# Optimization experiments

Measured on AMD Instinct MI355X. Metric: run time of the kernel, lower is better.

The kernel has to match this reference:

```python
import jax, jax.numpy as jnp
import numpy as np

B, L, D, H, NB = 8, 256, 128, 4, 2
HD = D // H
N_ITEMS, TIME_SPAN = 50000, 256
EPS = 1e-8
NEG = -(2.0 ** 32) + 1.0  # torch uses -2**32+1 padding value


def _ln(x, g, b):
    m = jnp.mean(x, -1, keepdims=True)
    v = jnp.mean((x - m) ** 2, -1, keepdims=True)
    return (x - m) / jnp.sqrt(v + EPS) * g + b


def setup_inputs() -> dict:
    ks = iter(jax.random.split(jax.random.key(0), 40))

    def nrm(shape, s=0.02):
        return jax.random.normal(next(ks), shape, jnp.float32) * s

    inp = {
        "user_ids": jax.random.randint(next(ks), (B,), 0, 1000),
        "log_seqs": jax.random.randint(next(ks), (B, L), 0, N_ITEMS + 1),
        "time_matrices": jax.random.randint(next(ks), (B, L, L), 0, TIME_SPAN + 1),
        "pos_seqs": jax.random.randint(next(ks), (B, L), 1, N_ITEMS + 1),
        "neg_seqs": jax.random.randint(next(ks), (B, L), 1, N_ITEMS + 1),
    }
    inp["item_emb"] = nrm((N_ITEMS + 1, D)).at[0].set(0.0)  # padding_idx=0
    inp["posK_emb"] = nrm((L, D))
    inp["posV_emb"] = nrm((L, D))
    inp["timeK_emb"] = nrm((TIME_SPAN + 1, D))
    inp["timeV_emb"] = nrm((TIME_SPAN + 1, D))
    inp["ln1_g"] = jnp.ones((NB, D)); inp["ln1_b"] = jnp.zeros((NB, D))
    inp["Wq"] = nrm((NB, D, D)); inp["bq"] = jnp.zeros((NB, D))
    inp["Wk"] = nrm((NB, D, D)); inp["bk"] = jnp.zeros((NB, D))
    inp["Wv"] = nrm((NB, D, D)); inp["bv"] = jnp.zeros((NB, D))
    inp["ln2_g"] = jnp.ones((NB, D)); inp["ln2_b"] = jnp.zeros((NB, D))
    inp["W1"] = nrm((NB, D, D)); inp["b1"] = jnp.zeros((NB, D))
    inp["W2"] = nrm((NB, D, D)); inp["b2"] = jnp.zeros((NB, D))
    inp["lnf_g"] = jnp.ones((D,)); inp["lnf_b"] = jnp.zeros((D,))
    return inp


def reference(user_ids, log_seqs, time_matrices, pos_seqs, neg_seqs,
              item_emb, posK_emb, posV_emb, timeK_emb, timeV_emb,
              ln1_g, ln1_b, Wq, bq, Wk, bk, Wv, bv, ln2_g, ln2_b,
              W1, b1, W2, b2, lnf_g, lnf_b):
    # dropout layers are identity in eval mode
    seqs = item_emb[log_seqs] * jnp.sqrt(jnp.float32(D))          # [B,L,D]
    tK = timeK_emb[time_matrices].reshape(B, L, L, H, HD)          # [B,Lq,Lk,H,hd]
    tV = timeV_emb[time_matrices].reshape(B, L, L, H, HD)
    pad = log_seqs == 0                                            # [B,L]
    seqs = seqs * (~pad)[..., None]
    causal = jnp.triu(jnp.ones((L, L), bool), 1)                   # ~tril -> masked
    # time_mask masks by QUERY position (matches torch unsqueeze(-1).expand)
    mask = pad[:, None, :, None] | causal[None, None]              # [B,1,Lq,Lk]
    posKh = posK_emb.reshape(L, H, HD)
    posVh = posV_emb.reshape(L, H, HD)
    for i in range(NB):
        q_in = _ln(seqs, ln1_g[i], ln1_b[i])
        Qh = (q_in @ Wq[i] + bq[i]).reshape(B, L, H, HD).transpose(0, 2, 1, 3)
        Kh = (seqs @ Wk[i] + bk[i]).reshape(B, L, H, HD).transpose(0, 2, 1, 3)
        Vh = (seqs @ Wv[i] + bv[i]).reshape(B, L, H, HD).transpose(0, 2, 1, 3)
        scores = jnp.einsum("bhqd,bhkd->bhqk", Qh, Kh)
        scores = scores + jnp.einsum("bhqd,khd->bhqk", Qh, posKh)
        scores = scores + jnp.einsum("bqkhd,bhqd->bhqk", tK, Qh)
        scores = scores / jnp.sqrt(jnp.float32(HD))
        scores = jnp.where(mask, NEG, scores)
        A = jax.nn.softmax(scores, axis=-1)                        # [B,H,Lq,Lk]
        out = jnp.einsum("bhqk,bhkd->bhqd", A, Vh)
        out = out + jnp.einsum("bhqk,khd->bhqd", A, posVh)
        out = out + jnp.einsum("bhqk,bqkhd->bhqd", A, tV)
        out = out.transpose(0, 2, 1, 3).reshape(B, L, D)
        seqs = q_in + out                                          # residual on Q
        seqs = _ln(seqs, ln2_g[i], ln2_b[i])
        h = jax.nn.relu(seqs @ W1[i] + b1[i])                      # conv1d k=1 == linear
        seqs = seqs + (h @ W2[i] + b2[i])
        seqs = seqs * (~pad)[..., None]
    feats = _ln(seqs, lnf_g, lnf_b)
    pos_logits = jnp.sum(feats * item_emb[pos_seqs], -1)           # [B,L]
    neg_logits = jnp.sum(feats * item_emb[neg_seqs], -1)
    return (pos_logits, neg_logits)
```

## Files before the change

kernel.cpp:

```cpp
#include <hip/hip_runtime.h>
#include <hip/hip_bf16.h>

#define L_ 256
#define H_ 4
#define ROWS 2048
#define NEGV (-4294967295.0f)

typedef unsigned short us16;

__device__ __forceinline__ float us2f(us16 u){ return __uint_as_float(((unsigned)u)<<16); }
__device__ __forceinline__ us16 f2us(float f){ __hip_bfloat16 h=__float2bfloat16(f); return *(us16*)&h; }

struct KArgs {
    const int *log_seqs, *tmat, *pos_seqs, *neg_seqs;
    const float *item_emb, *posK, *posV, *timeK, *timeV;
    const float *ln1g, *ln1b, *bq, *bk, *bv, *ln2g, *ln2b, *b1, *b2, *lnfg, *lnfb;
    const float *Wq, *Wk, *Wv, *W1, *W2;
    float *qin0, *qin1, *out;
    us16 *wsW, *tmK, *tmV, *Qb0, *Kb0, *Vb0, *Qb1, *Kb1, *Vb1;
};

__device__ __forceinline__ void ln_rows(float* sA,
        const float* __restrict__ g, const float* __restrict__ b,
        float* qin_out, int r0, int tid){
    int r=tid>>5, l=tid&31;
    float* x=sA+r*128;
    float x0=x[l],x1=x[l+32],x2=x[l+64],x3=x[l+96];
    float s=x0+x1+x2+x3;
    #pragma unroll
    for(int o=16;o;o>>=1) s+=__shfl_xor(s,o,64);
    float m=s*(1.f/128.f);
    float d0=x0-m,d1=x1-m,d2=x2-m,d3=x3-m;
    float v=d0*d0+d1*d1+d2*d2+d3*d3;
    #pragma unroll
    for(int o=16;o;o>>=1) v+=__shfl_xor(v,o,64);
    float rstd=rsqrtf(v*(1.f/128.f)+1e-8f);
    float y0=d0*rstd*g[l]+b[l];
    float y1=d1*rstd*g[l+32]+b[l+32];
    float y2=d2*rstd*g[l+64]+b[l+64];
    float y3=d3*rstd*g[l+96]+b[l+96];
    x[l]=y0; x[l+32]=y1; x[l+64]=y2; x[l+96]=y3;
    if(qin_out){
        float* q=qin_out+(size_t)(r0+r)*128;
        q[l]=y0; q[l+32]=y1; q[l+64]=y2; q[l+96]=y3;
    }
}

__device__ __forceinline__ void gemm2x2(const float* A, const us16* sW,
        int ra, int rb, int c0, float* acc){
    float a00=0,a01=0,a10=0,a11=0;
    const float* Ar=A+ra*128;
    const float* Br=A+rb*128;
    #pragma unroll 8
    for(int k=0;k<128;k++){
        ushort2 wp=*(const ushort2*)(sW+k*128+c0);
        float w0=us2f(wp.x), w1=us2f(wp.y);
        float x0=Ar[k], x1=Br[k];
        a00=fmaf(x0,w0,a00); a01=fmaf(x0,w1,a01);
        a10=fmaf(x1,w0,a10); a11=fmaf(x1,w1,a11);
    }
    acc[0]=a00; acc[1]=a01; acc[2]=a10; acc[3]=a11;
}

__global__ __launch_bounds__(256) void k_pre(KArgs a){
    __shared__ __align__(16) char smem[36864];
    int tid=threadIdx.x, bid=blockIdx.x;
    if(bid<768){
        us16* sW=(us16*)smem;
        float* sA=(float*)(smem+32768);
        int m=bid>>8, rg=bid&255, r0=rg*8;
        {
            int rl=tid>>5, c4=tid&31;
            int id=a.log_seqs[r0+rl];
            float4 v=((const float4*)a.item_emb)[id*32+c4];
            float sc = id? 11.3137085f : 0.f;
            v.x*=sc; v.y*=sc; v.z*=sc; v.w*=sc;
            ((float4*)sA)[tid]=v;
        }
        const float* Wsrc=(m==0)?a.Wq:(m==1)?a.Wk:a.Wv;
        {
            const float4* src=(const float4*)Wsrc;
            ushort4* dst=(ushort4*)sW;
            #pragma unroll
            for(int j=0;j<16;j++){
                float4 w=src[j*256+tid];
                ushort4 o; o.x=f2us(w.x);o.y=f2us(w.y);o.z=f2us(w.z);o.w=f2us(w.w);
                dst[j*256+tid]=o;
            }
        }
        __syncthreads();
        if(m==0){ ln_rows(sA, a.ln1g, a.ln1b, a.qin0, r0, tid); __syncthreads(); }
        int cp=tid&63, rp=tid>>6, c0=2*cp, ra=2*rp, rb=ra+1;
        float acc[4];
        gemm2x2(sA,sW,ra,rb,c0,acc);
        if(m==0){
            float b0v=a.bq[c0], b1v=a.bq[c0+1];
            ushort2 s0; s0.x=f2us(acc[0]+b0v); s0.y=f2us(acc[1]+b1v);
            ushort2 s1; s1.x=f2us(acc[2]+b0v); s1.y=f2us(acc[3]+b1v);
            *(ushort2*)(a.Qb0+(size_t)(r0+ra)*128+c0)=s0;
            *(ushort2*)(a.Qb0+(size_t)(r0+rb)*128+c0)=s1;
        } else {
            const float* bb=(m==1)?a.bk:a.bv;
            const float* pp=(m==1)?a.posK:a.posV;
            us16* Oo=(m==1)?a.Kb0:a.Vb0;
            int qa=(r0+ra)&255, qb2=(r0+rb)&255;
            float b0v=bb[c0], b1v=bb[c0+1];
            ushort2 s0; s0.x=f2us(acc[0]+b0v+pp[qa*128+c0]);  s0.y=f2us(acc[1]+b1v+pp[qa*128+c0+1]);
            ushort2 s1; s1.x=f2us(acc[2]+b0v+pp[qb2*128+c0]); s1.y=f2us(acc[3]+b1v+pp[qb2*128+c0+1]);
            *(ushort2*)(Oo+(size_t)(r0+ra)*128+c0)=s0;
            *(ushort2*)(Oo+(size_t)(r0+rb)*128+c0)=s1;
        }
    } else if(bid<880){
        int j=bid-768; int m=j>>4; int idx=(j&15)*256+tid;
        const float* base;
        switch(m){
            case 0: base=a.W1; break;        case 1: base=a.W2; break;
            case 2: base=a.Wq+16384; break;  case 3: base=a.Wk+16384; break;
            case 4: base=a.Wv+16384; break;  case 5: base=a.W1+16384; break;
            default: base=a.W2+16384; break;
        }
        float4 v=((const float4*)base)[idx];
        ushort4 o; o.x=f2us(v.x);o.y=f2us(v.y);o.z=f2us(v.z);o.w=f2us(v.w);
        ((ushort4*)(a.wsW+(size_t)m*16384))[idx]=o;
    } else {
        int gi=(bid-880)*256+tid;
        if(gi<8224){
            float4 v=((const float4*)a.timeK)[gi];
            ushort4 o; o.x=f2us(v.x);o.y=f2us(v.y);o.z=f2us(v.z);o.w=f2us(v.w);
            ((ushort4*)a.tmK)[gi]=o;
        } else if(gi<16448){
            int g2=gi-8224;
            float4 v=((const float4*)a.timeV)[g2];
            ushort4 o; o.x=f2us(v.x);o.y=f2us(v.y);o.z=f2us(v.z);o.w=f2us(v.w);
            ((ushort4*)a.tmV)[g2]=o;
        }
    }
}

__device__ __forceinline__ void stage_w512(const us16* __restrict__ Wg, us16* sW, int tid){
    const uint4* src=(const uint4*)Wg;
    uint4* dst=(uint4*)sW;
    #pragma unroll
    for(int j=0;j<4;j++) dst[j*512+tid]=src[j*512+tid];
}

__device__ __forceinline__ float gemv_half(const us16* sW, const float* x, int kh, int cc){
    float acc=0;
    int k0=kh*64;
    #pragma unroll 16
    for(int j=0;j<64;j++)
        acc=fmaf(x[k0+j], us2f(sW[(size_t)(k0+j)*128+cc]), acc);
    return acc;
}

__global__ __launch_bounds__(512,6) void k_blk(KArgs a, int layer){
    __shared__ __align__(16) char smem[38912];
    float* sQ  =(float*)smem;
    float* sS  =(float*)(smem+1024);
    us16*  sTMu=(us16*)(smem+9216);
    float* sPr =(float*)(smem+10240);
    float* sRed=(float*)(smem+26624);
    float* sRed2=(float*)(smem+26640);
    us16*  sW  =(us16*)smem;
    float* sX  =(float*)(smem+32768);
    float* sH  =(float*)(smem+33792);
    float* sY  =(float*)(smem+34816);
    float* sPart=(float*)(smem+35840);
    float* sRB =(float*)(smem+37888);

    int tid=threadIdx.x, bid=blockIdx.x;
    int b=bid>>7, p=bid&127;
    int q1=p, q2=255-p, b0=b*L_;
    int r1=b0+q1, r2=b0+q2;
    bool pad1=a.log_seqs[r1]==0, pad2=a.log_seqs[r2]==0;
    const us16* Qb = layer? a.Qb1:a.Qb0;
    const us16* Kb = layer? a.Kb1:a.Kb0;
    const us16* Vb = layer? a.Vb1:a.Vb0;
    const float* qin = layer? a.qin1:a.qin0;
    const float scale=0.17677669529663687f;
    if(tid<256){
        int i2=tid>>7, l=tid&127;
        sQ[tid]=us2f(Qb[(size_t)(i2?r2:r1)*128+l])*scale;
    }
    int i2g=tid>>8, kg=tid&255;
    int rg_ = i2g? r2:r1;
    int tmg = a.tmat[(size_t)rg_*L_+kg];
    sTMu[i2g*256+kg]=(us16)tmg;
    __syncthreads();

    {
        int qq = i2g? q2:q1; bool pad = i2g? pad2:pad1;
        bool act=(kg<=qq)&&!pad;
        float acc[4]={0.f,0.f,0.f,0.f};
        if(act){
            const uint4* K4=(const uint4*)(Kb+(size_t)(b0+kg)*128);
            const uint4* T4=(const uint4*)(a.tmK+(size_t)tmg*128);
            const float4* Q4=(const float4*)(sQ+i2g*128);
            #pragma unroll 4
            for(int c=0;c<16;c++){
                uint4 kv=K4[c]; uint4 tv=T4[c];
                float4 qa=Q4[2*c], qb=Q4[2*c+1];
                const us16* ku=(const us16*)&kv;
                const us16* tu=(const us16*)&tv;
                acc[c>>2]+= qa.x*(us2f(ku[0])+us2f(tu[0]))
                          + qa.y*(us2f(ku[1])+us2f(tu[1]))
                          + qa.z*(us2f(ku[2])+us2f(tu[2]))
                          + qa.w*(us2f(ku[3])+us2f(tu[3]))
                          + qb.x*(us2f(ku[4])+us2f(tu[4]))
                          + qb.y*(us2f(ku[5])+us2f(tu[5]))
                          + qb.z*(us2f(ku[6])+us2f(tu[6]))
                          + qb.w*(us2f(ku[7])+us2f(tu[7]));
            }
        }
        #pragma unroll
        for(int h=0;h<H_;h++) sS[(i2g*4+h)*256+kg]= act? acc[h]:NEGV;
    }
    __syncthreads();

    {
        int w=tid>>6, lane=tid&63;
        float* row=sS+w*256;
        float v0=row[lane],v1=row[lane+64],v2=row[lane+128],v3=row[lane+192];
        float mm=fmaxf(fmaxf(v0,v1),fmaxf(v2,v3));
        #pragma unroll
        for(int o=32;o;o>>=1) mm=fmaxf(mm,__shfl_xor(mm,o,64));
        float e0=__expf(v0-mm),e1=__expf(v1-mm),e2=__expf(v2-mm),e3=__expf(v3-mm);
        float ss=e0+e1+e2+e3;
        #pragma unroll
        for(int o=32;o;o>>=1) ss+=__shfl_xor(ss,o,64);
        float inv=1.f/ss;
        row[lane]=e0*inv; row[lane+64]=e1*inv; row[lane+128]=e2*inv; row[lane+192]=e3*inv;
    }
    __syncthreads();

    {
        int i2=tid>>8, s16=(tid>>4)&15, dq=tid&15;
        int qq=i2?q2:q1; bool pad=i2?pad2:pad1;
        int kend=pad?L_:qq+1;
        int k0=s16*16;
        int kmax=kend-k0; kmax=kmax<0?0:(kmax>16?16:kmax);
        const float* row=sS+(i2*4+(dq>>2))*256;
        const us16* tmrow=sTMu+i2*256;
        float a0=0,a1=0,a2=0,a3=0,a4=0,a5=0,a6=0,a7=0;
        for(int kk=0;kk<kmax;kk++){
            int kx=k0+kk;
            float aa=row[kx];
            int tmk=tmrow[kx];
            uint4 v4=((const uint4*)(Vb+(size_t)(b0+kx)*128))[dq];
            uint4 t4=((const uint4*)(a.tmV+(size_t)tmk*128))[dq];
            const us16* vu=(const us16*)&v4;
            const us16* tu=(const us16*)&t4;
            a0=fmaf(aa,us2f(vu[0])+us2f(tu[0]),a0);
            a1=fmaf(aa,us2f(vu[1])+us2f(tu[1]),a1);
            a2=fmaf(aa,us2f(vu[2])+us2f(tu[2]),a2);
            a3=fmaf(aa,us2f(vu[3])+us2f(tu[3]),a3);
            a4=fmaf(aa,us2f(vu[4])+us2f(tu[4]),a4);
            a5=fmaf(aa,us2f(vu[5])+us2f(tu[5]),a5);
            a6=fmaf(aa,us2f(vu[6])+us2f(tu[6]),a6);
            a7=fmaf(aa,us2f(vu[7])+us2f(tu[7]),a7);
        }
        float* dst=sPr+(i2*16+s16)*128+dq*8;
        ((float4*)dst)[0]=make_float4(a0,a1,a2,a3);
        ((float4*)dst)[1]=make_float4(a4,a5,a6,a7);
    }
    __syncthreads();

    if(tid<256){
        int ii=tid>>7, l=tid&127;
        int rr = ii? r2:r1;
        float v=qin[(size_t)rr*128+l];
        #pragma unroll
        for(int sl=0;sl<16;sl++) v+=sPr[(ii*16+sl)*128+l];
        float s=v;
        #pragma unroll
        for(int o=32;o;o>>=1) s+=__shfl_xor(s,o,64);
        if((tid&63)==0) sRed[ii*2+((tid>>6)&1)]=s;
        __syncthreads();
        float m=(sRed[ii*2]+sRed[ii*2+1])*(1.f/128.f);
        float d=v-m;
        float vv=d*d;
        #pragma unroll
        for(int o=32;o;o>>=1) vv+=__shfl_xor(vv,o,64);
        if((tid&63)==0) sRed2[ii*2+((tid>>6)&1)]=vv;
        __syncthreads();
        float rstd=rsqrtf((sRed2[ii*2]+sRed2[ii*2+1])*(1.f/128.f)+1e-8f);
        sX[ii*128+l]=d*rstd*a.ln2g[layer*128+l]+a.ln2b[layer*128+l];
    } else { __syncthreads(); __syncthreads(); }
    __syncthreads();

    int out=tid&255, kh=tid>>8, ii=out>>7, cc=out&127;
    int rr = ii? r2:r1;
    int qown = ii? q2:q1;
    bool padown = ii? pad2:pad1;

    stage_w512(a.wsW+(size_t)(layer?5:0)*16384, sW, tid);
    __syncthreads();
    sPart[tid]=gemv_half(sW, sX+ii*128, kh, cc);
    __syncthreads();
    if(tid<256) sH[out]=fmaxf(sPart[tid]+sPart[tid+256]+a.b1[layer*128+cc],0.f);
    __syncthreads();
    stage_w512(a.wsW+(size_t)(layer?6:1)*16384, sW, tid);
    __syncthreads();
    sPart[tid]=gemv_half(sW, sH+ii*128, kh, cc);
    __syncthreads();
    float f=0.f;
    if(tid<256){
        f=sPart[tid]+sPart[tid+256]+a.b2[layer*128+cc]+sX[out];
        if(padown) f=0.f;
        sY[out]=f;
    }
    __syncthreads();

    if(layer==0){
        if(tid<256){
            float s=f;
            #pragma unroll
            for(int o=32;o;o>>=1) s+=__shfl_xor(s,o,64);
            if((tid&63)==0) sRB[ii*2+((tid>>6)&1)]=s;
            __syncthreads();
            float m=(sRB[ii*2]+sRB[ii*2+1])*(1.f/128.f);
            float d=f-m;
            float vv=d*d;
            #pragma unroll
            for(int o=32;o;o>>=1) vv+=__shfl_xor(vv,o,64);
            if((tid&63)==0) sRB[4+ii*2+((tid>>6)&1)]=vv;
            __syncthreads();
            float rstd=rsqrtf((sRB[4+ii*2]+sRB[5+ii*2])*(1.f/128.f)+1e-8f);
            float y1=d*rstd*a.ln1g[128+cc]+a.ln1b[128+cc];
            a.qin1[(size_t)rr*128+cc]=y1;
            sX[out]=y1;
        } else { __syncthreads(); __syncthreads(); }
        __syncthreads();
        stage_w512(a.wsW+(size_t)2*16384, sW, tid);
        __syncthreads();
        sPart[tid]=gemv_half(sW, sX+ii*128, kh, cc);
        __syncthreads();
        if(tid<256) a.Qb1[(size_t)rr*128+cc]=f2us(sPart[tid]+sPart[tid+256]+a.bq[128+cc]);
        __syncthreads();
        stage_w512(a.wsW+(size_t)3*16384, sW, tid);
        __syncthreads();
        sPart[tid]=gemv_half(sW, sY+ii*128, kh, cc);
        __syncthreads();
        if(tid<256) a.Kb1[(size_t)rr*128+cc]=f2us(sPart[tid]+sPart[tid+256]+a.bk[128+cc]+a.posK[qown*128+cc]);
        __syncthreads();
        stage_w512(a.wsW+(size_t)4*16384, sW, tid);
        __syncthreads();
        sPart[tid]=gemv_half(sW, sY+ii*128, kh, cc);
        __syncthreads();
        if(tid<256) a.Vb1[(size_t)rr*128+cc]=f2us(sPart[tid]+sPart[tid+256]+a.bv[128+cc]+a.posV[qown*128+cc]);
    } else {
        if(tid<256){
            float s=f;
            #pragma unroll
            for(int o=32;o;o>>=1) s+=__shfl_xor(s,o,64);
            if((tid&63)==0) sRB[ii*2+((tid>>6)&1)]=s;
            __syncthreads();
            float m=(sRB[ii*2]+sRB[ii*2+1])*(1.f/128.f);
            float d=f-m;
            float vv=d*d;
            #pragma unroll
            for(int o=32;o;o>>=1) vv+=__shfl_xor(vv,o,64);
            if((tid&63)==0) sRB[4+ii*2+((tid>>6)&1)]=vv;
            __syncthreads();
            float rstd=rsqrtf((sRB[4+ii*2]+sRB[5+ii*2])*(1.f/128.f)+1e-8f);
            sX[out]=d*rstd*a.lnfg[cc]+a.lnfb[cc];
        } else { __syncthreads(); __syncthreads(); }
        __syncthreads();
        int w=tid>>6, lane=tid&63;
        if(w<4){
            int rowi=w>>1, neg=w&1;
            int rg = rowi? r2:r1;
            int id = neg? a.neg_seqs[rg] : a.pos_seqs[rg];
            const float* e=a.item_emb+(size_t)id*128;
            float s2 = sX[rowi*128+lane]*e[lane] + sX[rowi*128+lane+64]*e[lane+64];
            #pragma unroll
            for(int o=32;o;o>>=1) s2+=__shfl_xor(s2,o,64);
            if(lane==0) a.out[neg*ROWS+rg]=s2;
        }
    }
}

extern "C" void kernel_launch(void* const* d_in, const int* in_sizes, int n_in,
                              void* d_out, int out_size, void* d_ws, size_t ws_size,
                              hipStream_t stream) {
    KArgs a;
    a.log_seqs=(const int*)d_in[1];
    a.tmat    =(const int*)d_in[2];
    a.pos_seqs=(const int*)d_in[3];
    a.neg_seqs=(const int*)d_in[4];
    a.item_emb=(const float*)d_in[5];
    a.posK =(const float*)d_in[6];
    a.posV =(const float*)d_in[7];
    a.timeK=(const float*)d_in[8];
    a.timeV=(const float*)d_in[9];
    a.ln1g=(const float*)d_in[10];
    a.ln1b=(const float*)d_in[11];
    a.Wq=(const float*)d_in[12];
    a.bq=(const float*)d_in[13];
    a.Wk=(const float*)d_in[14];
    a.bk=(const float*)d_in[15];
    a.Wv=(const float*)d_in[16];
    a.bv=(const float*)d_in[17];
    a.ln2g=(const float*)d_in[18];
    a.ln2b=(const float*)d_in[19];
    a.W1=(const float*)d_in[20];
    a.b1=(const float*)d_in[21];
    a.W2=(const float*)d_in[22];
    a.b2=(const float*)d_in[23];
    a.lnfg=(const float*)d_in[24];
    a.lnfb=(const float*)d_in[25];

    const size_t MB=1u<<20;
    char* w=(char*)d_ws;
    a.qin0=(float*)(w+0*MB);
    a.qin1=(float*)(w+1*MB);
    a.Qb0 =(us16*) (w+2*MB);
    a.Kb0 =(us16*) (w+2*MB+512*1024);
    a.Vb0 =(us16*) (w+3*MB);
    a.Qb1 =(us16*) (w+3*MB+512*1024);
    a.Kb1 =(us16*) (w+4*MB);
    a.Vb1 =(us16*) (w+4*MB+512*1024);
    a.wsW =(us16*) (w+5*MB);
    a.tmK =(us16*) (w+5*MB+256*1024);
    a.tmV =(us16*) (w+5*MB+384*1024);
    a.out =(float*)d_out;

    k_pre<<<946,256,0,stream>>>(a);
    k_blk<<<1024,512,0,stream>>>(a,0);
    k_blk<<<1024,512,0,stream>>>(a,1);
}
```

Before: 231.3 us.

## Split attention over key halves with flash-style merge, separate FFN and QKV kernels

Attention is split across two key halves per query pair. Each half writes partial PV sums plus its softmax max and sum, and a new combine+FFN kernel merges the halves with log-sum-exp rescaling. The fused per-layer block kernel, which ran serial GEMVs over 2 rows with 512 threads, is replaced by separate FFN and QKV kernels that process 4 or 8 rows per block and load each staged weight once per block. This raises parallelism and weight reuse, at the cost of more launches and global round-trips for the partials.

```diff
diff --git a/kernel.cpp b/kernel.cpp
--- a/kernel.cpp
+++ b/kernel.cpp
@@ -16,7 +16,7 @@
     const float *item_emb, *posK, *posV, *timeK, *timeV;
     const float *ln1g, *ln1b, *bq, *bk, *bv, *ln2g, *ln2b, *b1, *b2, *lnfg, *lnfb;
     const float *Wq, *Wk, *Wv, *W1, *W2;
-    float *qin0, *qin1, *out;
+    float *qin0, *qin1, *seqs1, *PVp, *MSp, *out;
     us16 *wsW, *tmK, *tmV, *Qb0, *Kb0, *Vb0, *Qb1, *Kb1, *Vb1;
 };
 
@@ -62,6 +62,26 @@
     acc[0]=a00; acc[1]=a01; acc[2]=a10; acc[3]=a11;
 }
 
+__device__ __forceinline__ void gemm1x2(const float* Ar, const us16* sW,
+        int c0, float& o0, float& o1){
+    float a0=0,a1=0;
+    #pragma unroll 8
+    for(int k=0;k<128;k++){
+        ushort2 wp=*(const ushort2*)(sW+k*128+c0);
+        float x=Ar[k];
+        a0=fmaf(x,us2f(wp.x),a0);
+        a1=fmaf(x,us2f(wp.y),a1);
+    }
+    o0=a0; o1=a1;
+}
+
+__device__ __forceinline__ void stage_w(const us16* __restrict__ Wg, us16* sW, int tid){
+    const uint4* src=(const uint4*)Wg;
+    uint4* dst=(uint4*)sW;
+    #pragma unroll
+    for(int j=0;j<8;j++) dst[j*256+tid]=src[j*256+tid];
+}
+
 __global__ __launch_bounds__(256) void k_pre(KArgs a){
     __shared__ __align__(16) char smem[36864];
     int tid=threadIdx.x, bid=blockIdx.x;
@@ -137,55 +157,32 @@
     }
 }
 
-__device__ __forceinline__ void stage_w512(const us16* __restrict__ Wg, us16* sW, int tid){
-    const uint4* src=(const uint4*)Wg;
-    uint4* dst=(uint4*)sW;
-    #pragma unroll
-    for(int j=0;j<4;j++) dst[j*512+tid]=src[j*512+tid];
-}
-
-__device__ __forceinline__ float gemv_half(const us16* sW, const float* x, int kh, int cc){
-    float acc=0;
-    int k0=kh*64;
-    #pragma unroll 16
-    for(int j=0;j<64;j++)
-        acc=fmaf(x[k0+j], us2f(sW[(size_t)(k0+j)*128+cc]), acc);
-    return acc;
-}
-
-__global__ __launch_bounds__(512,6) void k_blk(KArgs a, int layer){
-    __shared__ __align__(16) char smem[38912];
+__global__ __launch_bounds__(256,8) void k_attnp(KArgs a, int layer){
+    __shared__ __align__(16) char smem[14080];
     float* sQ  =(float*)smem;
     float* sS  =(float*)(smem+1024);
-    us16*  sTMu=(us16*)(smem+9216);
-    float* sPr =(float*)(smem+10240);
-    float* sRed=(float*)(smem+26624);
-    float* sRed2=(float*)(smem+26640);
-    us16*  sW  =(us16*)smem;
-    float* sX  =(float*)(smem+32768);
-    float* sH  =(float*)(smem+33792);
-    float* sY  =(float*)(smem+34816);
-    float* sPart=(float*)(smem+35840);
-    float* sRB =(float*)(smem+37888);
+    us16*  sTM =(us16*)(smem+5120);
+    float* sPr =(float*)(smem+5632);
+    float* sMS =(float*)(smem+13824);
 
     int tid=threadIdx.x, bid=blockIdx.x;
-    int b=bid>>7, p=bid&127;
-    int q1=p, q2=255-p, b0=b*L_;
+    int qp=bid&127, kh=(bid>>7)&1, b=bid>>8;
+    int q1=qp, q2=255-qp, b0=b*L_;
     int r1=b0+q1, r2=b0+q2;
+    int k0=kh*128;
     bool pad1=a.log_seqs[r1]==0, pad2=a.log_seqs[r2]==0;
     const us16* Qb = layer? a.Qb1:a.Qb0;
     const us16* Kb = layer? a.Kb1:a.Kb0;
     const us16* Vb = layer? a.Vb1:a.Vb0;
-    const float* qin = layer? a.qin1:a.qin0;
     const float scale=0.17677669529663687f;
-    if(tid<256){
+    {
         int i2=tid>>7, l=tid&127;
-        sQ[tid]=us2f(Qb[(size_t)(i2?r2:r1)*128+l])*scale;
-    }
-    int i2g=tid>>8, kg=tid&255;
-    int rg_ = i2g? r2:r1;
-    int tmg = a.tmat[(size_t)rg_*L_+kg];
-    sTMu[i2g*256+kg]=(us16)tmg;
+        sQ[i2*128+l]=us2f(Qb[(size_t)(i2?r2:r1)*128+l])*scale;
+    }
+    int i2g=tid>>7, kk=tid&127, kg=k0+kk;
+    int rgr = i2g? r2:r1;
+    int tmg = a.tmat[(size_t)rgr*L_+kg];
+    sTM[i2g*128+kk]=(us16)tmg;
     __syncthreads();
 
     {
@@ -213,40 +210,45 @@
             }
         }
         #pragma unroll
-        for(int h=0;h<H_;h++) sS[(i2g*4+h)*256+kg]= act? acc[h]:NEGV;
+        for(int h=0;h<H_;h++) sS[(i2g*4+h)*128+kk]= act? acc[h]:NEGV;
     }
     __syncthreads();
 
     {
         int w=tid>>6, lane=tid&63;
-        float* row=sS+w*256;
-        float v0=row[lane],v1=row[lane+64],v2=row[lane+128],v3=row[lane+192];
-        float mm=fmaxf(fmaxf(v0,v1),fmaxf(v2,v3));
-        #pragma unroll
-        for(int o=32;o;o>>=1) mm=fmaxf(mm,__shfl_xor(mm,o,64));
-        float e0=__expf(v0-mm),e1=__expf(v1-mm),e2=__expf(v2-mm),e3=__expf(v3-mm);
-        float ss=e0+e1+e2+e3;
-        #pragma unroll
-        for(int o=32;o;o>>=1) ss+=__shfl_xor(ss,o,64);
-        float inv=1.f/ss;
-        row[lane]=e0*inv; row[lane+64]=e1*inv; row[lane+128]=e2*inv; row[lane+192]=e3*inv;
-    }
-    __syncthreads();
-
-    {
-        int i2=tid>>8, s16=(tid>>4)&15, dq=tid&15;
+        #pragma unroll
+        for(int rr=0;rr<2;rr++){
+            int row=w*2+rr;
+            float* rp_=sS+row*128;
+            float v0=rp_[lane], v1=rp_[lane+64];
+            float mm=fmaxf(v0,v1);
+            #pragma unroll
+            for(int o=32;o;o>>=1) mm=fmaxf(mm,__shfl_xor(mm,o,64));
+            float e0=__expf(v0-mm), e1=__expf(v1-mm);
+            float ss=e0+e1;
+            #pragma unroll
+            for(int o=32;o;o>>=1) ss+=__shfl_xor(ss,o,64);
+            rp_[lane]=e0; rp_[lane+64]=e1;
+            if(lane==0){ sMS[row*2]=mm; sMS[row*2+1]=ss; }
+        }
+    }
+    __syncthreads();
+
+    {
+        int i2=tid>>7, s8=(tid>>4)&7, dq=tid&15, hh=dq>>2;
         int qq=i2?q2:q1; bool pad=i2?pad2:pad1;
-        int kend=pad?L_:qq+1;
-        int k0=s16*16;
-        int kmax=kend-k0; kmax=kmax<0?0:(kmax>16?16:kmax);
-        const float* row=sS+(i2*4+(dq>>2))*256;
-        const us16* tmrow=sTMu+i2*256;
+        int kendg = pad? L_ : qq+1;
+        int kend = kendg - k0; kend = kend<0?0:(kend>128?128:kend);
+        int kk0=s8*16;
+        int kmax=kend-kk0; kmax=kmax<0?0:(kmax>16?16:kmax);
+        const float* row=sS+(i2*4+hh)*128;
+        const us16* tmrow=sTM+i2*128;
         float a0=0,a1=0,a2=0,a3=0,a4=0,a5=0,a6=0,a7=0;
-        for(int kk=0;kk<kmax;kk++){
-            int kx=k0+kk;
+        for(int kq=0;kq<kmax;kq++){
+            int kx=kk0+kq;
             float aa=row[kx];
             int tmk=tmrow[kx];
-            uint4 v4=((const uint4*)(Vb+(size_t)(b0+kx)*128))[dq];
+            uint4 v4=((const uint4*)(Vb+(size_t)(b0+k0+kx)*128))[dq];
             uint4 t4=((const uint4*)(a.tmV+(size_t)tmk*128))[dq];
             const us16* vu=(const us16*)&v4;
             const us16* tu=(const us16*)&t4;
@@ -259,123 +261,145 @@
             a6=fmaf(aa,us2f(vu[6])+us2f(tu[6]),a6);
             a7=fmaf(aa,us2f(vu[7])+us2f(tu[7]),a7);
         }
-        float* dst=sPr+(i2*16+s16)*128+dq*8;
+        float* dst=sPr+(i2*8+s8)*128+dq*8;
         ((float4*)dst)[0]=make_float4(a0,a1,a2,a3);
         ((float4*)dst)[1]=make_float4(a4,a5,a6,a7);
     }
     __syncthreads();
 
-    if(tid<256){
-        int ii=tid>>7, l=tid&127;
-        int rr = ii? r2:r1;
-        float v=qin[(size_t)rr*128+l];
-        #pragma unroll
-        for(int sl=0;sl<16;sl++) v+=sPr[(ii*16+sl)*128+l];
-        float s=v;
+    {
+        int i2=tid>>7, l=tid&127;
+        float pv=0;
+        #pragma unroll
+        for(int s=0;s<8;s++) pv+=sPr[(i2*8+s)*128+l];
+        a.PVp[(size_t)bid*256 + i2*128 + l]=pv;
+        if(tid<16) a.MSp[(size_t)bid*16+tid]=sMS[tid];
+    }
+}
+
+__global__ __launch_bounds__(256) void k_qkv(KArgs a){
+    __shared__ __align__(16) char smem[36864];
+    us16* sW=(us16*)smem;
+    float* sA=(float*)(smem+32768);
+    int tid=threadIdx.x;
+    int m=blockIdx.x>>8, rg=blockIdx.x&255, r0=rg*8;
+    ((float4*)sA)[tid]=((const float4*)(a.seqs1+(size_t)r0*128))[tid];
+    stage_w(a.wsW+(size_t)(2+m)*16384, sW, tid);
+    __syncthreads();
+    if(m==0){ ln_rows(sA, a.ln1g+128, a.ln1b+128, a.qin1, r0, tid); __syncthreads(); }
+    int cp=tid&63, rp=tid>>6, c0=2*cp, ra=2*rp, rb=ra+1;
+    float acc[4];
+    gemm2x2(sA,sW,ra,rb,c0,acc);
+    if(m==0){
+        float b0v=a.bq[128+c0], b1v=a.bq[128+c0+1];
+        ushort2 s0; s0.x=f2us(acc[0]+b0v); s0.y=f2us(acc[1]+b1v);
+        ushort2 s1; s1.x=f2us(acc[2]+b0v); s1.y=f2us(acc[3]+b1v);
+        *(ushort2*)(a.Qb1+(size_t)(r0+ra)*128+c0)=s0;
+        *(ushort2*)(a.Qb1+(size_t)(r0+rb)*128+c0)=s1;
+    } else {
+        const float* bb=(m==1)?(a.bk+128):(a.bv+128);
+        const float* pp=(m==1)?a.posK:a.posV;
+        us16* Oo=(m==1)?a.Kb1:a.Vb1;
+        int qa=(r0+ra)&255, qb2=(r0+rb)&255;
+        float b0v=bb[c0], b1v=bb[c0+1];
+        ushort2 s0; s0.x=f2us(acc[0]+b0v+pp[qa*128+c0]);  s0.y=f2us(acc[1]+b1v+pp[qa*128+c0+1]);
+        ushort2 s1; s1.x=f2us(acc[2]+b0v+pp[qb2*128+c0]); s1.y=f2us(acc[3]+b1v+pp[qb2*128+c0+1]);
+        *(ushort2*)(Oo+(size_t)(r0+ra)*128+c0)=s0;
+        *(ushort2*)(Oo+(size_t)(r0+rb)*128+c0)=s1;
+    }
+}
+
+__global__ __launch_bounds__(256) void k_cffn(KArgs a, int layer, int final_,
+                                              int slotW1, int slotW2){
+    __shared__ __align__(16) char smem[36864];
+    us16* sW=(us16*)smem;
+    float* sA=(float*)(smem+32768);
+    float* sH=(float*)(smem+34816);
+    int tid=threadIdx.x;
+    int r0=blockIdx.x*4;
+    int rp=tid>>6, lane=tid&63;
+    int r=r0+rp;
+    int b=r>>8, q=r&255;
+    int i2=(q>=128)?1:0;
+    int qp=i2? 255-q : q;
+    const float* qin = layer? a.qin1:a.qin0;
+    bool pad = a.log_seqs[r]==0;
+    size_t blk0=(size_t)(b*256+qp), blk1=(size_t)(b*256+128+qp);
+    stage_w(a.wsW+(size_t)slotW1*16384, sW, tid);
+
+    float o0,o1;
+    {
+        int d=lane; int h=d>>5;
+        float m0=a.MSp[blk0*16+(i2*4+h)*2],   s0=a.MSp[blk0*16+(i2*4+h)*2+1];
+        float m1=a.MSp[blk1*16+(i2*4+h)*2],   s1=a.MSp[blk1*16+(i2*4+h)*2+1];
+        float M=fmaxf(m0,m1);
+        float w0=__expf(m0-M), w1=__expf(m1-M);
+        float pv=w0*a.PVp[blk0*256+i2*128+d]+w1*a.PVp[blk1*256+i2*128+d];
+        o0=pv/(w0*s0+w1*s1)+qin[(size_t)r*128+d];
+    }
+    {
+        int d=lane+64; int h=d>>5;
+        float m0=a.MSp[blk0*16+(i2*4+h)*2],   s0=a.MSp[blk0*16+(i2*4+h)*2+1];
+        float m1=a.MSp[blk1*16+(i2*4+h)*2],   s1=a.MSp[blk1*16+(i2*4+h)*2+1];
+        float M=fmaxf(m0,m1);
+        float w0=__expf(m0-M), w1=__expf(m1-M);
+        float pv=w0*a.PVp[blk0*256+i2*128+d]+w1*a.PVp[blk1*256+i2*128+d];
+        o1=pv/(w0*s0+w1*s1)+qin[(size_t)r*128+d];
+    }
+    {
+        float s=o0+o1;
         #pragma unroll
         for(int o=32;o;o>>=1) s+=__shfl_xor(s,o,64);
-        if((tid&63)==0) sRed[ii*2+((tid>>6)&1)]=s;
+        float m=s*(1.f/128.f);
+        float d0=o0-m, d1=o1-m;
+        float v=d0*d0+d1*d1;
+        #pragma unroll
+        for(int o=32;o;o>>=1) v+=__shfl_xor(v,o,64);
+        float rstd=rsqrtf(v*(1.f/128.f)+1e-8f);
+        sA[rp*128+lane]   =d0*rstd*a.ln2g[layer*128+lane]+a.ln2b[layer*128+lane];
+        sA[rp*128+lane+64]=d1*rstd*a.ln2g[layer*128+lane+64]+a.ln2b[layer*128+lane+64];
+    }
+    __syncthreads();
+    int c0=2*lane;
+    float h0,h1;
+    gemm1x2(sA+rp*128, sW, c0, h0, h1);
+    sH[rp*128+c0]  =fmaxf(h0+a.b1[layer*128+c0],0.f);
+    sH[rp*128+c0+1]=fmaxf(h1+a.b1[layer*128+c0+1],0.f);
+    __syncthreads();
+    stage_w(a.wsW+(size_t)slotW2*16384, sW, tid);
+    __syncthreads();
+    float f0,f1;
+    gemm1x2(sH+rp*128, sW, c0, f0, f1);
+    f0 = pad?0.f:(f0+a.b2[layer*128+c0]  +sA[rp*128+c0]);
+    f1 = pad?0.f:(f1+a.b2[layer*128+c0+1]+sA[rp*128+c0+1]);
+    if(!final_){
+        a.seqs1[(size_t)r*128+c0]=f0;
+        a.seqs1[(size_t)r*128+c0+1]=f1;
+    } else {
         __syncthreads();
-        float m=(sRed[ii*2]+sRed[ii*2+1])*(1.f/128.f);
-        float d=v-m;
-        float vv=d*d;
-        #pragma unroll
-        for(int o=32;o;o>>=1) vv+=__shfl_xor(vv,o,64);
-        if((tid&63)==0) sRed2[ii*2+((tid>>6)&1)]=vv;
+        sA[rp*128+c0]=f0; sA[rp*128+c0+1]=f1;
         __syncthreads();
-        float rstd=rsqrtf((sRed2[ii*2]+sRed2[ii*2+1])*(1.f/128.f)+1e-8f);
-        sX[ii*128+l]=d*rstd*a.ln2g[layer*128+l]+a.ln2b[layer*128+l];
-    } else { __syncthreads(); __syncthreads(); }
-    __syncthreads();
-
-    int out=tid&255, kh=tid>>8, ii=out>>7, cc=out&127;
-    int rr = ii? r2:r1;
-    int qown = ii? q2:q1;
-    bool padown = ii? pad2:pad1;
-
-    stage_w512(a.wsW+(size_t)(layer?5:0)*16384, sW, tid);
-    __syncthreads();
-    sPart[tid]=gemv_half(sW, sX+ii*128, kh, cc);
-    __syncthreads();
-    if(tid<256) sH[out]=fmaxf(sPart[tid]+sPart[tid+256]+a.b1[layer*128+cc],0.f);
-    __syncthreads();
-    stage_w512(a.wsW+(size_t)(layer?6:1)*16384, sW, tid);
-    __syncthreads();
-    sPart[tid]=gemv_half(sW, sH+ii*128, kh, cc);
-    __syncthreads();
-    float f=0.f;
-    if(tid<256){
-        f=sPart[tid]+sPart[tid+256]+a.b2[layer*128+cc]+sX[out];
-        if(padown) f=0.f;
-        sY[out]=f;
-    }
-    __syncthreads();
-
-    if(layer==0){
-        if(tid<256){
-            float s=f;
+        float x0=sA[rp*128+lane], x1=sA[rp*128+lane+64];
+        float s=x0+x1;
+        #pragma unroll
+        for(int o=32;o;o>>=1) s+=__shfl_xor(s,o,64);
+        float m=s*(1.f/128.f);
+        float d0=x0-m, d1=x1-m;
+        float v=d0*d0+d1*d1;
+        #pragma unroll
+        for(int o=32;o;o>>=1) v+=__shfl_xor(v,o,64);
+        float rstd=rsqrtf(v*(1.f/128.f)+1e-8f);
+        float y0=d0*rstd*a.lnfg[lane]+a.lnfb[lane];
+        float y1=d1*rstd*a.lnfg[lane+64]+a.lnfb[lane+64];
+        sH[rp*128+lane]=y0; sH[rp*128+lane+64]=y1;
+        #pragma unroll
+        for(int neg=0;neg<2;neg++){
+            int id = neg? a.neg_seqs[r] : a.pos_seqs[r];
+            const float* e=a.item_emb+(size_t)id*128;
+            float sd = sH[rp*128+lane]*e[lane] + sH[rp*128+lane+64]*e[lane+64];
             #pragma unroll
-            for(int o=32;o;o>>=1) s+=__shfl_xor(s,o,64);
-            if((tid&63)==0) sRB[ii*2+((tid>>6)&1)]=s;
-            __syncthreads();
-            float m=(sRB[ii*2]+sRB[ii*2+1])*(1.f/128.f);
-            float d=f-m;
-            float vv=d*d;
-            #pragma unroll
-            for(int o=32;o;o>>=1) vv+=__shfl_xor(vv,o,64);
-            if((tid&63)==0) sRB[4+ii*2+((tid>>6)&1)]=vv;
-            __syncthreads();
-            float rstd=rsqrtf((sRB[4+ii*2]+sRB[5+ii*2])*(1.f/128.f)+1e-8f);
-            float y1=d*rstd*a.ln1g[128+cc]+a.ln1b[128+cc];
-            a.qin1[(size_t)rr*128+cc]=y1;
-            sX[out]=y1;
-        } else { __syncthreads(); __syncthreads(); }
-        __syncthreads();
-        stage_w512(a.wsW+(size_t)2*16384, sW, tid);
-        __syncthreads();
-        sPart[tid]=gemv_half(sW, sX+ii*128, kh, cc);
-        __syncthreads();
-        if(tid<256) a.Qb1[(size_t)rr*128+cc]=f2us(sPart[tid]+sPart[tid+256]+a.bq[128+cc]);
-        __syncthreads();
-        stage_w512(a.wsW+(size_t)3*16384, sW, tid);
-        __syncthreads();
-        sPart[tid]=gemv_half(sW, sY+ii*128, kh, cc);
-        __syncthreads();
-        if(tid<256) a.Kb1[(size_t)rr*128+cc]=f2us(sPart[tid]+sPart[tid+256]+a.bk[128+cc]+a.posK[qown*128+cc]);
-        __syncthreads();
-        stage_w512(a.wsW+(size_t)4*16384, sW, tid);
-        __syncthreads();
-        sPart[tid]=gemv_half(sW, sY+ii*128, kh, cc);
-        __syncthreads();
-        if(tid<256) a.Vb1[(size_t)rr*128+cc]=f2us(sPart[tid]+sPart[tid+256]+a.bv[128+cc]+a.posV[qown*128+cc]);
-    } else {
-        if(tid<256){
-            float s=f;
-            #pragma unroll
-            for(int o=32;o;o>>=1) s+=__shfl_xor(s,o,64);
-            if((tid&63)==0) sRB[ii*2+((tid>>6)&1)]=s;
-            __syncthreads();
-            float m=(sRB[ii*2]+sRB[ii*2+1])*(1.f/128.f);
-            float d=f-m;
-            float vv=d*d;
-            #pragma unroll
-            for(int o=32;o;o>>=1) vv+=__shfl_xor(vv,o,64);
-            if((tid&63)==0) sRB[4+ii*2+((tid>>6)&1)]=vv;
-            __syncthreads();
-            float rstd=rsqrtf((sRB[4+ii*2]+sRB[5+ii*2])*(1.f/128.f)+1e-8f);
-            sX[out]=d*rstd*a.lnfg[cc]+a.lnfb[cc];
-        } else { __syncthreads(); __syncthreads(); }
-        __syncthreads();
-        int w=tid>>6, lane=tid&63;
-        if(w<4){
-            int rowi=w>>1, neg=w&1;
-            int rg = rowi? r2:r1;
-            int id = neg? a.neg_seqs[rg] : a.pos_seqs[rg];
-            const float* e=a.item_emb+(size_t)id*128;
-            float s2 = sX[rowi*128+lane]*e[lane] + sX[rowi*128+lane+64]*e[lane+64];
-            #pragma unroll
-            for(int o=32;o;o>>=1) s2+=__shfl_xor(s2,o,64);
-            if(lane==0) a.out[neg*ROWS+rg]=s2;
+            for(int o=32;o;o>>=1) sd+=__shfl_xor(sd,o,64);
+            if(lane==0) a.out[neg*ROWS+r]=sd;
         }
     }
 }
@@ -412,20 +436,26 @@
 
     const size_t MB=1u<<20;
     char* w=(char*)d_ws;
-    a.qin0=(float*)(w+0*MB);
-    a.qin1=(float*)(w+1*MB);
-    a.Qb0 =(us16*) (w+2*MB);
-    a.Kb0 =(us16*) (w+2*MB+512*1024);
-    a.Vb0 =(us16*) (w+3*MB);
-    a.Qb1 =(us16*) (w+3*MB+512*1024);
-    a.Kb1 =(us16*) (w+4*MB);
-    a.Vb1 =(us16*) (w+4*MB+512*1024);
-    a.wsW =(us16*) (w+5*MB);
-    a.tmK =(us16*) (w+5*MB+256*1024);
-    a.tmV =(us16*) (w+5*MB+384*1024);
-    a.out =(float*)d_out;
-
-    k_pre<<<946,256,0,stream>>>(a);
-    k_blk<<<1024,512,0,stream>>>(a,0);
-    k_blk<<<1024,512,0,stream>>>(a,1);
-}
+    a.qin0 =(float*)(w+0*MB);
+    a.qin1 =(float*)(w+1*MB);
+    a.Qb0  =(us16*) (w+2*MB);
+    a.Kb0  =(us16*) (w+2*MB+512*1024);
+    a.Vb0  =(us16*) (w+3*MB);
+    a.Qb1  =(us16*) (w+3*MB+512*1024);
+    a.Kb1  =(us16*) (w+4*MB);
+    a.Vb1  =(us16*) (w+4*MB+512*1024);
+    a.wsW  =(us16*) (w+5*MB);
+    a.tmK  =(us16*) (w+5*MB+256*1024);
+    a.tmV  =(us16*) (w+5*MB+384*1024);
+    a.PVp  =(float*)(w+6*MB);
+    a.MSp  =(float*)(w+8*MB+512*1024);
+    a.seqs1=(float*)(w+9*MB);
+    a.out  =(float*)d_out;
+
+    k_pre  <<<946 ,256,0,stream>>>(a);
+    k_attnp<<<2048,256,0,stream>>>(a,0);
+    k_cffn <<<512 ,256,0,stream>>>(a,0,0, 0,1);
+    k_qkv  <<<768 ,256,0,stream>>>(a);
+    k_attnp<<<2048,256,0,stream>>>(a,1);
+    k_cffn <<<512 ,256,0,stream>>>(a,1,1, 5,6);
+}
```

Result: slower. 244.0 us (+5.5%).
